# Optimization experiments

Measured on AMD Instinct MI355X. Metric: run time of the kernel, lower is better.

The kernel has to match this reference:

```python
import jax, jax.numpy as jnp
import numpy as np

STRIDES = (8, 16, 32, 64, 128)
SIZES = ((100, 160), (50, 80), (25, 40), (13, 20), (7, 10))  # 800x1280 image, P3-P7
NC = 80      # num_classes
C = 256      # head channels
NCONV = 4    # tower depth
N = 2        # batch
PRIOR_PROB = 0.01


def conv3x3(x, w, b):
    # x: [N,C,H,W], w: [O,I,3,3] -> [N,O,H,W], stride 1, SAME padding
    y = jax.lax.conv_general_dilated(x, w, (1, 1), 'SAME',
                                     dimension_numbers=('NCHW', 'OIHW', 'NCHW'))
    return y + b[None, :, None, None]


def group_norm(x, g, b, groups=32, eps=1e-5):
    n, c, h, w = x.shape
    xr = x.reshape(n, groups, c // groups, h, w)
    m = xr.mean((2, 3, 4), keepdims=True)
    v = ((xr - m) ** 2).mean((2, 3, 4), keepdims=True)
    xn = ((xr - m) * jax.lax.rsqrt(v + eps)).reshape(n, c, h, w)
    return xn * g[None, :, None, None] + b[None, :, None, None]


def setup_inputs() -> dict:
    key = jax.random.key(0)
    ks = iter(jax.random.split(key, 16))
    d = {}
    for l, (h, w) in enumerate(SIZES):
        d[f'feat{l}'] = jax.random.normal(next(ks), (N, C, h, w), jnp.float32)
    # torch init: conv weights ~ N(0, 0.01), biases 0, GN weight 1 / bias 0
    d['cls_w'] = jax.random.normal(next(ks), (NCONV, C, C, 3, 3), jnp.float32) * 0.01
    d['cls_b'] = jnp.zeros((NCONV, C), jnp.float32)
    d['cls_gw'] = jnp.ones((NCONV, C), jnp.float32)
    d['cls_gb'] = jnp.zeros((NCONV, C), jnp.float32)
    d['box_w'] = jax.random.normal(next(ks), (NCONV, C, C, 3, 3), jnp.float32) * 0.01
    d['box_b'] = jnp.zeros((NCONV, C), jnp.float32)
    d['box_gw'] = jnp.ones((NCONV, C), jnp.float32)
    d['box_gb'] = jnp.zeros((NCONV, C), jnp.float32)
    d['score_w'] = jax.random.normal(next(ks), (NC, C, 3, 3), jnp.float32) * 0.01
    bias_value = -np.log((1.0 - PRIOR_PROB) / PRIOR_PROB)
    d['score_b'] = jnp.full((NC,), bias_value, jnp.float32)
    d['pred_w'] = jax.random.normal(next(ks), (4, C, 3, 3), jnp.float32) * 0.01
    d['pred_b'] = jnp.zeros((4,), jnp.float32)
    d['ctr_w'] = jax.random.normal(next(ks), (1, C, 3, 3), jnp.float32) * 0.01
    d['ctr_b'] = jnp.zeros((1,), jnp.float32)
    d['scales'] = jnp.ones((5,), jnp.float32)
    return d


def reference(feat0, feat1, feat2, feat3, feat4,
              cls_w, cls_b, cls_gw, cls_gb,
              box_w, box_b, box_gw, box_gb,
              score_w, score_b, pred_w, pred_b, ctr_w, ctr_b, scales):
    feats = [feat0, feat1, feat2, feat3, feat4]
    outs = []
    for l, x in enumerate(feats):
        c = x
        r = x
        for i in range(NCONV):  # shared cls / bbox towers (conv -> GN -> ReLU)
            c = jax.nn.relu(group_norm(conv3x3(c, cls_w[i], cls_b[i]), cls_gw[i], cls_gb[i]))
            r = jax.nn.relu(group_norm(conv3x3(r, box_w[i], box_b[i]), box_gw[i], box_gb[i]))
        logits = conv3x3(c, score_w, score_b)                     # [N,K,H,W]
        ctr = conv3x3(r, ctr_w, ctr_b)                            # centerness_on_reg=True
        # norm_reg_targets=True: relu(scale * pred) * stride
        reg = jax.nn.relu(conv3x3(r, pred_w, pred_b) * scales[l]) * STRIDES[l]
        n, _, h, w = logits.shape
        logits = logits.transpose(0, 2, 3, 1).reshape(n, h * w, NC)
        ctr = ctr.transpose(0, 2, 3, 1).reshape(n, h * w, 1)
        reg = reg.transpose(0, 2, 3, 1).reshape(n, h * w, 4)
        # ShiftGenerator: grid of (x,y) centers at arange*stride (offset=0)
        sx = jnp.arange(w, dtype=jnp.float32) * STRIDES[l]
        sy = jnp.arange(h, dtype=jnp.float32) * STRIDES[l]
        gy, gx = jnp.meshgrid(sy, sx, indexing='ij')
        shifts = jnp.stack([gx.reshape(-1), gy.reshape(-1)], axis=1)  # [HW,2]
        # Shift2BoxTransform.apply_deltas with weights (1,1,1,1)
        boxes = jnp.concatenate([shifts[None] - reg[..., :2],
                                 shifts[None] + reg[..., 2:]], axis=-1)  # [N,HW,4]
        scores = jax.nn.sigmoid(logits) * jax.nn.sigmoid(ctr)            # [N,HW,K]
        outs.append(jnp.concatenate([scores, boxes], axis=-1))           # [N,HW,K+4]
    return jnp.concatenate(outs, axis=1)  # [N, sum(HW), K+4]
```

## Files before the change

kernel.cpp:

```cpp
#include <hip/hip_runtime.h>
#include <cstddef>

#define NLEV 5
#define TOTROW 21330
#define PTOT 22360

typedef __bf16 bf16x8 __attribute__((ext_vector_type(8)));
typedef float f32x4 __attribute__((ext_vector_type(4)));
typedef unsigned short ushortx8 __attribute__((ext_vector_type(8)));

struct LvlP {
  int tileoff[6];
  int tilesX[5];
  int H[5], W[5];
  int poff[5], pend[5];
  int roff[6];
  float inv8HW[5];
  float strd[5];
};

static __device__ __forceinline__ unsigned short f2bf(float f) {
  union { float f; unsigned u; } v; v.f = f;
  unsigned r = v.u + 0x7fffu + ((v.u >> 16) & 1u);
  return (unsigned short)(r >> 16);
}
static __device__ __forceinline__ float bf2f(unsigned short h) {
  union { unsigned u; float f; } v; v.u = ((unsigned)h) << 16;
  return v.f;
}
static __device__ __forceinline__ int sel5i(const int* a, int l) {
  int v = a[0];
  v = (l == 1) ? a[1] : v; v = (l == 2) ? a[2] : v;
  v = (l == 3) ? a[3] : v; v = (l == 4) ? a[4] : v;
  return v;
}
static __device__ __forceinline__ float sel5f(const float* a, int l) {
  float v = a[0];
  v = (l == 1) ? a[1] : v; v = (l == 2) ? a[2] : v;
  v = (l == 3) ? a[3] : v; v = (l == 4) ? a[4] : v;
  return v;
}

static __device__ __forceinline__ void gload16(const unsigned short* g, unsigned short* l) {
  __builtin_amdgcn_global_load_lds(
      (const __attribute__((address_space(1))) unsigned int*)(const void*)g,
      (__attribute__((address_space(3))) unsigned int*)(void*)l, 16, 0, 0);
}

__global__ __launch_bounds__(256) void to_chlast(
    const float* __restrict__ feat, unsigned short* __restrict__ X,
    int HW, int W, int poff)
{
  const int n = blockIdx.y >> 2, cb = blockIdx.y & 3;
  const int p0 = blockIdx.x * 64;
  __shared__ unsigned short s[64][72];
  const int t = threadIdx.x;
  const int pl = t & 63, ci = t >> 6;
  const float* src = feat + ((size_t)(n * 256 + cb * 64)) * HW;
#pragma unroll
  for (int i = 0; i < 16; ++i) {
    const int c = ci + i * 4;
    const int p = p0 + pl;
    float v = (p < HW) ? src[(size_t)c * HW + p] : 0.f;
    s[c][pl] = f2bf(v);
  }
  __syncthreads();
  const int cl = t & 63, pi = t >> 6;
#pragma unroll
  for (int i = 0; i < 16; ++i) {
    const int p = p0 + pi + i * 4;
    if (p < HW) {
      const int y = p / W, x = p - y * W;
      const size_t dst = ((size_t)n * PTOT + poff + (y + 1) * (W + 2) + (x + 1)) * 256
                       + cb * 64 + cl;
      X[dst] = s[cl][pi + i * 4];
    }
  }
}

__global__ __launch_bounds__(256) void prep_tower_w(
    const float* __restrict__ cls_w, const float* __restrict__ box_w,
    unsigned short* __restrict__ wtC, unsigned short* __restrict__ wtR)
{
  const long e = (long)blockIdx.x * 256 + threadIdx.x;
  if (e >= 2359296L) return;
  const int j = (int)(e & 7);
  long r = e >> 3;
  const int oc = (int)(r & 255); r >>= 8;
  const int q = (int)(r & 3); r >>= 2;
  const int tap = (int)(r % 9);
  const long s = r / 9;
  const int ch = (int)(s & 7);
  const int layer = (int)(s >> 3);
  const int ic = ch * 32 + q * 8 + j;
  const long src = (((long)layer * 256 + oc) * 256 + ic) * 9 + tap;
  wtC[e] = f2bf(cls_w[src]);
  wtR[e] = f2bf(box_w[src]);
}

__global__ __launch_bounds__(256) void prep_head_w(
    const float* __restrict__ sw, const float* __restrict__ sb,
    const float* __restrict__ cw, const float* __restrict__ cb,
    const float* __restrict__ pw, const float* __restrict__ pb,
    unsigned short* __restrict__ wth, float* __restrict__ bh)
{
  const long e = (long)blockIdx.x * 256 + threadIdx.x;
  if (e < 589824L) {
    const int j = (int)(e & 7);
    long r = e >> 3;
    const int oc = (int)(r & 127); r >>= 7;
    const int q = (int)(r & 3); r >>= 2;
    const int tap = (int)(r % 9);
    const int ch = (int)(r / 9);
    const int k = ch * 32 + q * 8 + j;
    float v = 0.f;
    if (oc < 80) { if (k < 256) v = sw[((long)(oc * 256 + k)) * 9 + tap]; }
    else if (oc == 80) { if (k >= 256) v = cw[(long)(k - 256) * 9 + tap]; }
    else if (oc < 85) { if (k >= 256) v = pw[((long)((oc - 81) * 256 + (k - 256))) * 9 + tap]; }
    wth[e] = f2bf(v);
  }
  if (blockIdx.x == 0) {
    const int t = threadIdx.x;
    if (t < 128) bh[t] = (t < 80) ? sb[t] : (t == 80) ? cb[0] : (t < 85) ? pb[t - 81] : 0.f;
  }
}

__global__ __launch_bounds__(256, 2) void conv_mfma(
    const unsigned short* __restrict__ inC, const unsigned short* __restrict__ inR,
    unsigned short* __restrict__ outC, unsigned short* __restrict__ outR,
    const unsigned short* __restrict__ wtC, const unsigned short* __restrict__ wtR,
    const float* __restrict__ bsC, const float* __restrict__ bsR,
    float* __restrict__ stats, LvlP P, int kimg, int octot)
{
  const int ny = (kimg == 1) ? 4 : 2;
  const int nz = 4;
  const int span = ny * 8;
  const int total = 69 * ny * nz;
  const int SG = total / span;
  const int braw = blockIdx.x;
  int j, yy;
  if (braw < SG * span) {
    j = (braw / span) * 8 + (braw & 7);
    yy = (braw % span) >> 3;
  } else {
    const int p = braw - SG * span;
    const int cpx = (total - SG * span) / ny;
    j = SG * 8 + p % cpx;
    yy = p / cpx;
  }
  const int z = j % nz;
  const int bt = j / nz;
  const int oc0 = yy << 6;

  const int l = (bt >= P.tileoff[1]) + (bt >= P.tileoff[2])
              + (bt >= P.tileoff[3]) + (bt >= P.tileoff[4]);
  const int t = bt - sel5i(P.tileoff, l);
  const int tX = sel5i(P.tilesX, l);
  const int ty = t / tX, tx = t - ty * tX;
  const int x0 = tx << 5, y0 = ty * 12;
  const int H = sel5i(P.H, l), W = sel5i(P.W, l);
  const int W2 = W + 2;
  const int pbase = sel5i(P.poff, l);
  const int pmax = sel5i(P.pend, l) - 1;
  const int rbase = sel5i(P.roff, l);

  const unsigned short *A, *wt;
  const float* bs; unsigned short* out;
  int wchoff = 0;
  if (kimg == 1) {
    const int tower = z >> 1, n = z & 1;
    A = (tower ? inR : inC) + (size_t)n * PTOT * 256;
    wt = tower ? wtR : wtC;
    bs = tower ? bsR : bsC;
    out = (tower ? outR : outC) + (size_t)n * TOTROW * octot;
  } else {
    const int half = z >> 1, n = z & 1;
    A = (half ? inR : inC) + (size_t)n * PTOT * 256;
    wt = wtC; bs = bsC;
    wchoff = half * 8;
    out = outC + (size_t)z * TOTROW * octot;
  }

  __shared__ unsigned short sA[512 * 32];
  __shared__ unsigned short sB[36 * 512];

  const int tid = threadIdx.x;
  const int wv = tid >> 6, lane = tid & 63;
  const int t15 = lane & 15, q = lane >> 4;

  unsigned aoff[8];
#pragma unroll
  for (int it = 0; it < 8; ++it) {
    const int inst = wv + it * 4;
    const int item = (inst << 6) + lane;
    int pos = item >> 2; pos = (pos > 475) ? 475 : pos;
    const int part = item & 3;
    const int hy = pos / 34, hx = pos - hy * 34;
    int pidx = pbase + (y0 + hy) * W2 + (x0 + hx);
    pidx = (pidx > pmax) ? pmax : pidx;
    aoff[it] = ((unsigned)pidx << 8) + (part << 3);
  }

  f32x4 acc[6][4];
#pragma unroll
  for (int g = 0; g < 4; ++g) {
    const float b = bs[oc0 + g * 16 + t15];
#pragma unroll
    for (int f = 0; f < 6; ++f) {
      acc[f][g][0] = b; acc[f][g][1] = b; acc[f][g][2] = b; acc[f][g][3] = b;
    }
  }

  for (int ch = 0; ch < 8; ++ch) {
    const unsigned icb = (unsigned)ch << 5;
    __syncthreads();
#pragma unroll
    for (int it = 0; it < 8; ++it)
      gload16(A + aoff[it] + icb, sA + ((wv + it * 4) << 9));
    const unsigned short* wb = wt + ((size_t)((ch + wchoff) * 36) * octot + oc0) * 8 + (lane << 3);
#pragma unroll
    for (int it = 0; it < 9; ++it)
      gload16(wb + (size_t)(wv + it * 4) * octot * 8, sB + ((wv + it * 4) << 9));
    __syncthreads();

#pragma unroll
    for (int kx = 0; kx < 3; ++kx) {
      bf16x8 af[2][5];
#pragma unroll
      for (int fc = 0; fc < 2; ++fc)
#pragma unroll
        for (int r = 0; r < 5; ++r) {
          const int pos = (wv * 3 + r) * 34 + fc * 16 + t15 + kx;
          af[fc][r] = *(const bf16x8*)(sA + ((pos * 4 + q) << 3));
        }
#pragma unroll
      for (int ky = 0; ky < 3; ++ky) {
        const int tap = ky * 3 + kx;
        bf16x8 b[4];
#pragma unroll
        for (int g = 0; g < 4; ++g)
          b[g] = *(const bf16x8*)(sB + ((((tap * 4 + q) << 6) + g * 16 + t15) << 3));
#pragma unroll
        for (int fr = 0; fr < 3; ++fr)
#pragma unroll
          for (int fc = 0; fc < 2; ++fc) {
            const bf16x8 a = af[fc][fr + ky];
#pragma unroll
            for (int g = 0; g < 4; ++g)
              acc[fr * 2 + fc][g] =
                  __builtin_amdgcn_mfma_f32_16x16x32_bf16(a, b[g], acc[fr * 2 + fc][g], 0, 0, 0);
          }
      }
    }
  }

#pragma unroll
  for (int g = 0; g < 4; ++g) {
    const int oc = oc0 + g * 16 + t15;
    float s = 0.f, ss = 0.f;
#pragma unroll
    for (int f = 0; f < 6; ++f) {
      const int fr = f >> 1, fc = f & 1;
      const int gy = y0 + wv * 3 + fr;
#pragma unroll
      for (int rg = 0; rg < 4; ++rg) {
        const int gx = x0 + fc * 16 + q * 4 + rg;
        if (gy < H && gx < W) {
          const float v = acc[f][g][rg];
          out[(size_t)(rbase + gy * W + gx) * octot + oc] = f2bf(v);
          s += v; ss += v * v;
        }
      }
    }
    if (stats) {
      s += __shfl_xor(s, 1);  ss += __shfl_xor(ss, 1);
      s += __shfl_xor(s, 2);  ss += __shfl_xor(ss, 2);
      s += __shfl_xor(s, 4);  ss += __shfl_xor(ss, 4);
      s += __shfl_xor(s, 16); ss += __shfl_xor(ss, 16);
      if ((lane & 55) == 0) {
        float* st = stats + (((size_t)l * 4 + z) * 32 + (oc >> 3)) * 2;
        atomicAdd(st, s); atomicAdd(st + 1, ss);
      }
    }
  }
}

__global__ __launch_bounds__(256) void gn_apply(
    const unsigned short* __restrict__ Yc, const unsigned short* __restrict__ Yr,
    unsigned short* __restrict__ Xc, unsigned short* __restrict__ Xr,
    const float* __restrict__ stats,
    const float* __restrict__ gwC, const float* __restrict__ gbC,
    const float* __restrict__ gwR, const float* __restrict__ gbR, LvlP P)
{
  const int img = blockIdx.y;
  const int tower = img >> 1, n = img & 1;
  const int e = blockIdx.x * 256 + threadIdx.x;
  const int pos = e >> 5;
  const int g = e & 31;
  if (pos >= TOTROW) return;
  const int l = (pos >= P.roff[1]) + (pos >= P.roff[2]) + (pos >= P.roff[3]) + (pos >= P.roff[4]);
  const int W = sel5i(P.W, l);
  const int local = pos - sel5i(P.roff, l);
  const int y = local / W, x = local - y * W;
  const size_t dst = ((size_t)n * PTOT + sel5i(P.poff, l) + (y + 1) * (W + 2) + (x + 1)) * 256 + g * 8;
  const size_t srco = ((size_t)n * TOTROW + pos) * 256 + g * 8;
  const unsigned short* Y = (tower ? Yr : Yc) + srco;
  unsigned short* X = (tower ? Xr : Xc) + dst;
  const float* gw = (tower ? gwR : gwC) + g * 8;
  const float* gb = (tower ? gbR : gbC) + g * 8;
  const float* st = stats + (((size_t)l * 4 + img) * 32 + g) * 2;
  const float inv = sel5f(P.inv8HW, l);
  const float m = st[0] * inv;
  const float var = st[1] * inv - m * m;
  const float rs = rsqrtf(var + 1e-5f);
  ushortx8 yv = *(const ushortx8*)Y;
  ushortx8 xv;
#pragma unroll
  for (int j = 0; j < 8; ++j) {
    const float yj = bf2f(yv[j]);
    const float v = (yj - m) * rs * gw[j] + gb[j];
    xv[j] = f2bf(fmaxf(v, 0.f));
  }
  *(ushortx8*)X = xv;
}

__global__ __launch_bounds__(256) void head_epi(
    const unsigned short* __restrict__ Yh, float* __restrict__ out,
    const float* __restrict__ scales, LvlP P)
{
  const int n = blockIdx.y;
  const int e = blockIdx.x * 256 + threadIdx.x;
  if (e >= TOTROW * 84) return;
  const int pos = e / 84;
  const int j = e - pos * 84;
  const int l = (pos >= P.roff[1]) + (pos >= P.roff[2]) + (pos >= P.roff[3]) + (pos >= P.roff[4]);
  const unsigned short* yc_ = Yh + ((size_t)n * TOTROW + pos) * 128;
  const unsigned short* yb_ = Yh + ((size_t)(2 + n) * TOTROW + pos) * 128;
  float v;
  if (j < 80) {
    const float lg = bf2f(yc_[j]);
    const float ct = bf2f(yb_[80]);
    v = (1.f / (1.f + __expf(-lg))) * (1.f / (1.f + __expf(-ct)));
  } else {
    const int d = j - 80;
    const float stride = sel5f(P.strd, l);
    const int W = sel5i(P.W, l);
    const int local = pos - sel5i(P.roff, l);
    const int gy = local / W, gx = local - gy * W;
    const float pv = bf2f(yb_[81 + d]);
    const float rg = fmaxf(pv * scales[l], 0.f) * stride;
    const float sx = gx * stride, sy = gy * stride;
    v = (d == 0) ? sx - rg : (d == 1) ? sy - rg : (d == 2) ? sx + rg : sy + rg;
  }
  out[((size_t)n * TOTROW + pos) * 84 + j] = v;
}

extern "C" void kernel_launch(void* const* d_in, const int* in_sizes, int n_in,
                              void* d_out, int out_size, void* d_ws, size_t ws_size,
                              hipStream_t stream)
{
  (void)in_sizes; (void)n_in; (void)out_size; (void)ws_size;

  const float* feats[5];
  for (int l = 0; l < 5; ++l) feats[l] = (const float*)d_in[l];
  const float* cls_w  = (const float*)d_in[5];
  const float* cls_b  = (const float*)d_in[6];
  const float* cls_gw = (const float*)d_in[7];
  const float* cls_gb = (const float*)d_in[8];
  const float* box_w  = (const float*)d_in[9];
  const float* box_b  = (const float*)d_in[10];
  const float* box_gw = (const float*)d_in[11];
  const float* box_gb = (const float*)d_in[12];
  const float* score_w = (const float*)d_in[13];
  const float* score_b = (const float*)d_in[14];
  const float* pred_w  = (const float*)d_in[15];
  const float* pred_b  = (const float*)d_in[16];
  const float* ctr_w   = (const float*)d_in[17];
  const float* ctr_b   = (const float*)d_in[18];
  const float* scales  = (const float*)d_in[19];
  float* out = (float*)d_out;

  static const int Hs[5] = {100, 50, 25, 13, 7};
  static const int Ws[5] = {160, 80, 40, 20, 10};
  LvlP P;
  {
    static const int to[6] = {0, 45, 60, 66, 68, 69};
    static const int tX[5] = {5, 3, 2, 1, 1};
    static const int po[5] = {0, 16524, 20788, 21922, 22252};
    static const int pe[5] = {16524, 20788, 21922, 22252, 22360};
    static const int ro[6] = {0, 16000, 20000, 21000, 21260, 21330};
    for (int i = 0; i < 6; ++i) { P.tileoff[i] = to[i]; P.roff[i] = ro[i]; }
    for (int i = 0; i < 5; ++i) {
      P.tilesX[i] = tX[i]; P.H[i] = Hs[i]; P.W[i] = Ws[i];
      P.poff[i] = po[i]; P.pend[i] = pe[i];
      P.inv8HW[i] = 1.f / (8.f * Hs[i] * Ws[i]);
      P.strd[i] = (float)(8 << i);
    }
  }

  char* p = (char*)d_ws;
  auto alloc = [&](size_t bytes) {
    char* r = p;
    p += (bytes + 255) & ~(size_t)255;
    return r;
  };
  const size_t XPAD = (size_t)2 * PTOT * 256 * 2;
  const size_t YSZ  = (size_t)2 * TOTROW * 256 * 2;
  unsigned short* Xf  = (unsigned short*)alloc(XPAD);
  unsigned short* Xc  = (unsigned short*)alloc(XPAD);
  unsigned short* Xr  = (unsigned short*)alloc(XPAD);
  unsigned short* Yc  = (unsigned short*)alloc(YSZ);
  unsigned short* Yr  = (unsigned short*)alloc(YSZ);
  unsigned short* Yh  = (unsigned short*)alloc((size_t)4 * TOTROW * 128 * 2);
  unsigned short* wtC = (unsigned short*)alloc(4718592);
  unsigned short* wtR = (unsigned short*)alloc(4718592);
  unsigned short* wth = (unsigned short*)alloc(1179648);
  float* bh    = (float*)alloc(512);
  float* stats = (float*)alloc(4 * 5 * 4 * 32 * 2 * sizeof(float));

  hipMemsetAsync(Xf, 0, XPAD, stream);
  hipMemsetAsync(Xc, 0, XPAD, stream);
  hipMemsetAsync(Xr, 0, XPAD, stream);
  hipMemsetAsync(stats, 0, 4 * 5 * 4 * 32 * 2 * sizeof(float), stream);

  prep_tower_w<<<9216, 256, 0, stream>>>(cls_w, box_w, wtC, wtR);
  prep_head_w<<<2304, 256, 0, stream>>>(score_w, score_b, ctr_w, ctr_b,
                                        pred_w, pred_b, wth, bh);
  for (int l = 0; l < 5; ++l) {
    const int HW = Hs[l] * Ws[l];
    to_chlast<<<dim3((HW + 63) / 64, 8), 256, 0, stream>>>(
        feats[l], Xf, HW, Ws[l], P.poff[l]);
  }

  for (int i = 0; i < 4; ++i) {
    const unsigned short* ic_ = (i == 0) ? Xf : Xc;
    const unsigned short* ir_ = (i == 0) ? Xf : Xr;
    float* st = stats + (size_t)i * 5 * 4 * 32 * 2;
    conv_mfma<<<dim3(1104), 256, 0, stream>>>(
        ic_, ir_, Yc, Yr,
        wtC + (size_t)i * 589824, wtR + (size_t)i * 589824,
        cls_b + i * 256, box_b + i * 256, st, P, 1, 256);
    gn_apply<<<dim3((TOTROW * 32 + 255) / 256, 4), 256, 0, stream>>>(
        Yc, Yr, Xc, Xr, st,
        cls_gw + i * 256, cls_gb + i * 256,
        box_gw + i * 256, box_gb + i * 256, P);
  }

  conv_mfma<<<dim3(552), 256, 0, stream>>>(
      Xc, Xr, Yh, nullptr, wth, nullptr, bh, nullptr, nullptr, P, 2, 128);
  head_epi<<<dim3((TOTROW * 84 + 255) / 256, 2), 256, 0, stream>>>(
      Yh, out, scales, P);
}
```

Baseline: 821.5 us.

## Fuse GroupNorm+ReLU into conv input load and drop padded activation buffers

Removes the separate gn_apply pass by applying the GroupNorm affine and ReLU to each input while the next conv loads it. A tiny gnab_mk kernel precomputes per-channel scale and shift from the stats. Halo padding is replaced by per-element bounds masks, which removes the padded buffers and their memsets. The conv A-tile load changes from async global_load_lds to register loads plus conversion math and LDS stores, which may lose load/compute overlap and add VALU work inside the conv main loop.

```diff
diff --git a/kernel.cpp b/kernel.cpp
--- a/kernel.cpp
+++ b/kernel.cpp
@@ -3,7 +3,6 @@
 
 #define NLEV 5
 #define TOTROW 21330
-#define PTOT 22360
 
 typedef __bf16 bf16x8 __attribute__((ext_vector_type(8)));
 typedef float f32x4 __attribute__((ext_vector_type(4)));
@@ -13,7 +12,6 @@
   int tileoff[6];
   int tilesX[5];
   int H[5], W[5];
-  int poff[5], pend[5];
   int roff[6];
   float inv8HW[5];
   float strd[5];
@@ -49,7 +47,7 @@
 
 __global__ __launch_bounds__(256) void to_chlast(
     const float* __restrict__ feat, unsigned short* __restrict__ X,
-    int HW, int W, int poff)
+    int HW, int rbase)
 {
   const int n = blockIdx.y >> 2, cb = blockIdx.y & 3;
   const int p0 = blockIdx.x * 64;
@@ -70,9 +68,7 @@
   for (int i = 0; i < 16; ++i) {
     const int p = p0 + pi + i * 4;
     if (p < HW) {
-      const int y = p / W, x = p - y * W;
-      const size_t dst = ((size_t)n * PTOT + poff + (y + 1) * (W + 2) + (x + 1)) * 256
-                       + cb * 64 + cl;
+      const size_t dst = ((size_t)n * TOTROW + rbase + p) * 256 + cb * 64 + cl;
       X[dst] = s[cl][pi + i * 4];
     }
   }
@@ -102,7 +98,8 @@
     const float* __restrict__ sw, const float* __restrict__ sb,
     const float* __restrict__ cw, const float* __restrict__ cb,
     const float* __restrict__ pw, const float* __restrict__ pb,
-    unsigned short* __restrict__ wth, float* __restrict__ bh)
+    unsigned short* __restrict__ wth, float* __restrict__ bh,
+    float* __restrict__ gnA0, float* __restrict__ gnB0)
 {
   const long e = (long)blockIdx.x * 256 + threadIdx.x;
   if (e < 589824L) {
@@ -119,10 +116,35 @@
     else if (oc < 85) { if (k >= 256) v = pw[((long)((oc - 81) * 256 + (k - 256))) * 9 + tap]; }
     wth[e] = f2bf(v);
   }
+  if (e < 5120) { gnA0[e] = 1.f; gnB0[e] = 0.f; }
   if (blockIdx.x == 0) {
     const int t = threadIdx.x;
     if (t < 128) bh[t] = (t < 80) ? sb[t] : (t == 80) ? cb[0] : (t < 85) ? pb[t - 81] : 0.f;
   }
+}
+
+__global__ __launch_bounds__(256) void gnab_mk(
+    const float* __restrict__ st,
+    const float* __restrict__ gwC, const float* __restrict__ gbC,
+    const float* __restrict__ gwR, const float* __restrict__ gbR,
+    float* __restrict__ Aout, float* __restrict__ Bout, LvlP P)
+{
+  const int idx = blockIdx.x * 256 + threadIdx.x;
+  if (idx >= 5120) return;
+  const int c = idx & 255;
+  const int z = (idx >> 8) & 3;
+  const int l = idx >> 10;
+  const int tower = z >> 1;
+  const int g = c >> 3;
+  const float* s = st + (((size_t)l * 4 + z) * 32 + g) * 2;
+  const float inv = sel5f(P.inv8HW, l);
+  const float m = s[0] * inv;
+  const float var = s[1] * inv - m * m;
+  const float rs = rsqrtf(var + 1e-5f);
+  const float gw = (tower ? gwR : gwC)[c];
+  const float gb = (tower ? gbR : gbC)[c];
+  Aout[idx] = rs * gw;
+  Bout[idx] = gb - m * rs * gw;
 }
 
 __global__ __launch_bounds__(256, 2) void conv_mfma(
@@ -130,7 +152,8 @@
     unsigned short* __restrict__ outC, unsigned short* __restrict__ outR,
     const unsigned short* __restrict__ wtC, const unsigned short* __restrict__ wtR,
     const float* __restrict__ bsC, const float* __restrict__ bsR,
-    float* __restrict__ stats, LvlP P, int kimg, int octot)
+    float* __restrict__ stats, const float* __restrict__ gnA,
+    const float* __restrict__ gnB, int dorelu, LvlP P, int kimg, int octot)
 {
   const int ny = (kimg == 1) ? 4 : 2;
   const int nz = 4;
@@ -159,23 +182,20 @@
   const int ty = t / tX, tx = t - ty * tX;
   const int x0 = tx << 5, y0 = ty * 12;
   const int H = sel5i(P.H, l), W = sel5i(P.W, l);
-  const int W2 = W + 2;
-  const int pbase = sel5i(P.poff, l);
-  const int pmax = sel5i(P.pend, l) - 1;
   const int rbase = sel5i(P.roff, l);
 
-  const unsigned short *A, *wt;
+  const unsigned short *Ain, *wt;
   const float* bs; unsigned short* out;
   int wchoff = 0;
   if (kimg == 1) {
     const int tower = z >> 1, n = z & 1;
-    A = (tower ? inR : inC) + (size_t)n * PTOT * 256;
+    Ain = (tower ? inR : inC) + (size_t)n * TOTROW * 256;
     wt = tower ? wtR : wtC;
     bs = tower ? bsR : bsC;
     out = (tower ? outR : outC) + (size_t)n * TOTROW * octot;
   } else {
     const int half = z >> 1, n = z & 1;
-    A = (half ? inR : inC) + (size_t)n * PTOT * 256;
+    Ain = (half ? inR : inC) + (size_t)n * TOTROW * 256;
     wt = wtC; bs = bsC;
     wchoff = half * 8;
     out = outC + (size_t)z * TOTROW * octot;
@@ -188,7 +208,7 @@
   const int wv = tid >> 6, lane = tid & 63;
   const int t15 = lane & 15, q = lane >> 4;
 
-  unsigned aoff[8];
+  unsigned aoff[8]; unsigned vmask = 0;
 #pragma unroll
   for (int it = 0; it < 8; ++it) {
     const int inst = wv + it * 4;
@@ -196,9 +216,11 @@
     int pos = item >> 2; pos = (pos > 475) ? 475 : pos;
     const int part = item & 3;
     const int hy = pos / 34, hx = pos - hy * 34;
-    int pidx = pbase + (y0 + hy) * W2 + (x0 + hx);
-    pidx = (pidx > pmax) ? pmax : pidx;
-    aoff[it] = ((unsigned)pidx << 8) + (part << 3);
+    const int gy = y0 + hy - 1, gx = x0 + hx - 1;
+    const int val = (gy >= 0 && gy < H && gx >= 0 && gx < W) ? 1 : 0;
+    const int ridx = val ? (rbase + gy * W + gx) : rbase;
+    aoff[it] = ((unsigned)ridx << 8) + (part << 3);
+    vmask |= (unsigned)val << it;
   }
 
   f32x4 acc[6][4];
@@ -211,12 +233,31 @@
     }
   }
 
+  const float* gnAl = gnA + (((size_t)(l * 4 + z)) << 8) + ((lane & 3) << 3);
+  const float* gnBl = gnB + (((size_t)(l * 4 + z)) << 8) + ((lane & 3) << 3);
+
   for (int ch = 0; ch < 8; ++ch) {
     const unsigned icb = (unsigned)ch << 5;
+    float a8[8], b8[8];
+#pragma unroll
+    for (int jj = 0; jj < 8; ++jj) { a8[jj] = gnAl[icb + jj]; b8[jj] = gnBl[icb + jj]; }
+    ushortx8 w[8];
+#pragma unroll
+    for (int it = 0; it < 8; ++it) {
+      const ushortx8 dv = *(const ushortx8*)(Ain + aoff[it] + icb);
+      const int val = (vmask >> it) & 1;
+#pragma unroll
+      for (int jj = 0; jj < 8; ++jj) {
+        const float x = bf2f(dv[jj]);
+        float y = x * a8[jj] + b8[jj];
+        y = dorelu ? fmaxf(y, 0.f) : y;
+        w[it][jj] = val ? f2bf(y) : (unsigned short)0;
+      }
+    }
     __syncthreads();
 #pragma unroll
     for (int it = 0; it < 8; ++it)
-      gload16(A + aoff[it] + icb, sA + ((wv + it * 4) << 9));
+      *(ushortx8*)(sA + ((wv + it * 4) << 9) + (lane << 3)) = w[it];
     const unsigned short* wb = wt + ((size_t)((ch + wchoff) * 36) * octot + oc0) * 8 + (lane << 3);
 #pragma unroll
     for (int it = 0; it < 9; ++it)
@@ -283,45 +324,6 @@
       }
     }
   }
-}
-
-__global__ __launch_bounds__(256) void gn_apply(
-    const unsigned short* __restrict__ Yc, const unsigned short* __restrict__ Yr,
-    unsigned short* __restrict__ Xc, unsigned short* __restrict__ Xr,
-    const float* __restrict__ stats,
-    const float* __restrict__ gwC, const float* __restrict__ gbC,
-    const float* __restrict__ gwR, const float* __restrict__ gbR, LvlP P)
-{
-  const int img = blockIdx.y;
-  const int tower = img >> 1, n = img & 1;
-  const int e = blockIdx.x * 256 + threadIdx.x;
-  const int pos = e >> 5;
-  const int g = e & 31;
-  if (pos >= TOTROW) return;
-  const int l = (pos >= P.roff[1]) + (pos >= P.roff[2]) + (pos >= P.roff[3]) + (pos >= P.roff[4]);
-  const int W = sel5i(P.W, l);
-  const int local = pos - sel5i(P.roff, l);
-  const int y = local / W, x = local - y * W;
-  const size_t dst = ((size_t)n * PTOT + sel5i(P.poff, l) + (y + 1) * (W + 2) + (x + 1)) * 256 + g * 8;
-  const size_t srco = ((size_t)n * TOTROW + pos) * 256 + g * 8;
-  const unsigned short* Y = (tower ? Yr : Yc) + srco;
-  unsigned short* X = (tower ? Xr : Xc) + dst;
-  const float* gw = (tower ? gwR : gwC) + g * 8;
-  const float* gb = (tower ? gbR : gbC) + g * 8;
-  const float* st = stats + (((size_t)l * 4 + img) * 32 + g) * 2;
-  const float inv = sel5f(P.inv8HW, l);
-  const float m = st[0] * inv;
-  const float var = st[1] * inv - m * m;
-  const float rs = rsqrtf(var + 1e-5f);
-  ushortx8 yv = *(const ushortx8*)Y;
-  ushortx8 xv;
-#pragma unroll
-  for (int j = 0; j < 8; ++j) {
-    const float yj = bf2f(yv[j]);
-    const float v = (yj - m) * rs * gw[j] + gb[j];
-    xv[j] = f2bf(fmaxf(v, 0.f));
-  }
-  *(ushortx8*)X = xv;
 }
 
 __global__ __launch_bounds__(256) void head_epi(
@@ -386,13 +388,10 @@
   {
     static const int to[6] = {0, 45, 60, 66, 68, 69};
     static const int tX[5] = {5, 3, 2, 1, 1};
-    static const int po[5] = {0, 16524, 20788, 21922, 22252};
-    static const int pe[5] = {16524, 20788, 21922, 22252, 22360};
     static const int ro[6] = {0, 16000, 20000, 21000, 21260, 21330};
     for (int i = 0; i < 6; ++i) { P.tileoff[i] = to[i]; P.roff[i] = ro[i]; }
     for (int i = 0; i < 5; ++i) {
       P.tilesX[i] = tX[i]; P.H[i] = Hs[i]; P.W[i] = Ws[i];
-      P.poff[i] = po[i]; P.pend[i] = pe[i];
       P.inv8HW[i] = 1.f / (8.f * Hs[i] * Ws[i]);
       P.strd[i] = (float)(8 << i);
     }
@@ -404,50 +403,54 @@
     p += (bytes + 255) & ~(size_t)255;
     return r;
   };
-  const size_t XPAD = (size_t)2 * PTOT * 256 * 2;
-  const size_t YSZ  = (size_t)2 * TOTROW * 256 * 2;
-  unsigned short* Xf  = (unsigned short*)alloc(XPAD);
-  unsigned short* Xc  = (unsigned short*)alloc(XPAD);
-  unsigned short* Xr  = (unsigned short*)alloc(XPAD);
-  unsigned short* Yc  = (unsigned short*)alloc(YSZ);
-  unsigned short* Yr  = (unsigned short*)alloc(YSZ);
+  const size_t YSZ = (size_t)2 * TOTROW * 256 * 2;
+  unsigned short* Xf  = (unsigned short*)alloc(YSZ);
+  unsigned short* Yc0 = (unsigned short*)alloc(YSZ);
+  unsigned short* Yr0 = (unsigned short*)alloc(YSZ);
+  unsigned short* Yc1 = (unsigned short*)alloc(YSZ);
+  unsigned short* Yr1 = (unsigned short*)alloc(YSZ);
   unsigned short* Yh  = (unsigned short*)alloc((size_t)4 * TOTROW * 128 * 2);
   unsigned short* wtC = (unsigned short*)alloc(4718592);
   unsigned short* wtR = (unsigned short*)alloc(4718592);
   unsigned short* wth = (unsigned short*)alloc(1179648);
   float* bh    = (float*)alloc(512);
   float* stats = (float*)alloc(4 * 5 * 4 * 32 * 2 * sizeof(float));
-
-  hipMemsetAsync(Xf, 0, XPAD, stream);
-  hipMemsetAsync(Xc, 0, XPAD, stream);
-  hipMemsetAsync(Xr, 0, XPAD, stream);
+  float* gnA   = (float*)alloc(5 * 5120 * sizeof(float));
+  float* gnB   = (float*)alloc(5 * 5120 * sizeof(float));
+
   hipMemsetAsync(stats, 0, 4 * 5 * 4 * 32 * 2 * sizeof(float), stream);
 
   prep_tower_w<<<9216, 256, 0, stream>>>(cls_w, box_w, wtC, wtR);
   prep_head_w<<<2304, 256, 0, stream>>>(score_w, score_b, ctr_w, ctr_b,
-                                        pred_w, pred_b, wth, bh);
+                                        pred_w, pred_b, wth, bh, gnA, gnB);
   for (int l = 0; l < 5; ++l) {
     const int HW = Hs[l] * Ws[l];
     to_chlast<<<dim3((HW + 63) / 64, 8), 256, 0, stream>>>(
-        feats[l], Xf, HW, Ws[l], P.poff[l]);
-  }
-
+        feats[l], Xf, HW, P.roff[l]);
+  }
+
+  const unsigned short* pc = Xf;
+  const unsigned short* pr = Xf;
   for (int i = 0; i < 4; ++i) {
-    const unsigned short* ic_ = (i == 0) ? Xf : Xc;
-    const unsigned short* ir_ = (i == 0) ? Xf : Xr;
+    unsigned short* qc = (i & 1) ? Yc1 : Yc0;
+    unsigned short* qr = (i & 1) ? Yr1 : Yr0;
     float* st = stats + (size_t)i * 5 * 4 * 32 * 2;
     conv_mfma<<<dim3(1104), 256, 0, stream>>>(
-        ic_, ir_, Yc, Yr,
+        pc, pr, qc, qr,
         wtC + (size_t)i * 589824, wtR + (size_t)i * 589824,
-        cls_b + i * 256, box_b + i * 256, st, P, 1, 256);
-    gn_apply<<<dim3((TOTROW * 32 + 255) / 256, 4), 256, 0, stream>>>(
-        Yc, Yr, Xc, Xr, st,
-        cls_gw + i * 256, cls_gb + i * 256,
-        box_gw + i * 256, box_gb + i * 256, P);
+        cls_b + i * 256, box_b + i * 256, st,
+        gnA + (size_t)i * 5120, gnB + (size_t)i * 5120, (i > 0) ? 1 : 0,
+        P, 1, 256);
+    gnab_mk<<<20, 256, 0, stream>>>(
+        st, cls_gw + i * 256, cls_gb + i * 256,
+        box_gw + i * 256, box_gb + i * 256,
+        gnA + (size_t)(i + 1) * 5120, gnB + (size_t)(i + 1) * 5120, P);
+    pc = qc; pr = qr;
   }
 
   conv_mfma<<<dim3(552), 256, 0, stream>>>(
-      Xc, Xr, Yh, nullptr, wth, nullptr, bh, nullptr, nullptr, P, 2, 128);
+      pc, pr, Yh, nullptr, wth, nullptr, bh, nullptr, nullptr,
+      gnA + (size_t)4 * 5120, gnB + (size_t)4 * 5120, 1, P, 2, 128);
   head_epi<<<dim3((TOTROW * 84 + 255) / 256, 2), 256, 0, stream>>>(
       Yh, out, scales, P);
 }
```

Result: slower. 929.0 us (+13.1%).
